# Kernel optimization log

Hardware: AMD Instinct MI355X
Metric: run time of the kernel (lower is better)

## Reference

```python
import jax, jax.numpy as jnp
import numpy as np

MIN_VAL = -1200.0
MAX_VAL = 1000.0


def setup_inputs() -> dict:
    key = jax.random.key(0)
    k1, _ = jax.random.split(key)
    # Scale so values spread across the [-1200, 1000] range; a small tail
    # falls outside the range and must be ignored (torch.histc semantics).
    x = jax.random.normal(k1, (32, 12, 256, 256), dtype=jnp.float32) * 400.0
    hist_counts = jnp.zeros((12, 2200), dtype=jnp.float32)
    return {"x": x, "hist_counts": hist_counts}


def reference(x, hist_counts):
    """Fused multi-channel histogram matching torch.histc per channel.

    torch.histc semantics: `bins` uniform bins over [min, max]; values
    outside [min, max] are ignored; values exactly equal to max land in the
    last bin. Returns updated hist_counts (buffer + batch histogram).
    """
    C, bins = hist_counts.shape
    # [B, C, H, W] -> [C, B*H*W]
    xf = jnp.transpose(x, (1, 0, 2, 3)).reshape(C, -1).astype(jnp.float32)
    scale = bins / (MAX_VAL - MIN_VAL)
    idx = jnp.floor((xf - MIN_VAL) * scale).astype(jnp.int32)
    idx = jnp.clip(idx, 0, bins - 1)  # maps x == MAX_VAL into last bin
    in_range = (xf >= MIN_VAL) & (xf <= MAX_VAL)
    # Flatten channel+bin into one scatter; out-of-range -> dump slot C*bins.
    flat_idx = idx + jnp.arange(C, dtype=jnp.int32)[:, None] * bins
    flat_idx = jnp.where(in_range, flat_idx, C * bins)
    counts = jnp.zeros(C * bins + 1, dtype=jnp.float32).at[flat_idx.ravel()].add(1.0)
    return hist_counts + counts[: C * bins].reshape(C, bins)
```

## Files before the change

### kernel.cpp

```cpp
#include <hip/hip_runtime.h>

#define NCHAN 12
#define NBINS 2200
#define HMIN  (-1200.0f)
#define HMAX  (1000.0f)
#define SLICE_ELEMS 65536
#define SPLIT 4
#define BLOCK 256

__global__ __launch_bounds__(BLOCK)
void init_out(const float* __restrict__ hist, float* __restrict__ out, int n) {
    int i = (blockIdx.x * BLOCK + threadIdx.x) * 4;
    if (i + 3 < n) {
        *(float4*)(out + i) = *(const float4*)(hist + i);
    } else {
        for (; i < n; ++i) out[i] = hist[i];
    }
}

__device__ __forceinline__ void bin4(const float4 v, unsigned int* lh) {
    float vals[4] = {v.x, v.y, v.z, v.w};
#pragma unroll
    for (int j = 0; j < 4; ++j) {
        float t = vals[j] + 1200.0f;
        if (t >= 0.0f && vals[j] <= HMAX) {
            int idx = min((int)t, NBINS - 1);
            atomicAdd(&lh[idx], 1u);
        }
    }
}

__global__ __launch_bounds__(BLOCK)
void hist_kernel(const float* __restrict__ x, float* __restrict__ out) {
    __shared__ unsigned int lh[NBINS];
    for (int i = threadIdx.x; i < NBINS; i += BLOCK) lh[i] = 0u;
    __syncthreads();

    const int slice = blockIdx.x / SPLIT;
    const int sub   = blockIdx.x % SPLIT;
    const int c     = slice % NCHAN;
    const int chunk = SLICE_ELEMS / SPLIT;

    const float4* __restrict__ xp =
        (const float4*)(x + (long long)slice * SLICE_ELEMS + (long long)sub * chunk);

#pragma unroll
    for (int k = 0; k < 2; ++k) {
        const int base = threadIdx.x + k * (BLOCK * 8);
        float4 v[8];
#pragma unroll
        for (int u = 0; u < 8; ++u) v[u] = xp[base + u * BLOCK];
#pragma unroll
        for (int u = 0; u < 8; ++u) bin4(v[u], lh);
    }
    __syncthreads();

    float* __restrict__ outc = out + c * NBINS;
    for (int i = threadIdx.x; i < NBINS; i += BLOCK) {
        unsigned int v = lh[i];
        if (v) atomicAdd(&outc[i], (float)v);
    }
}

extern "C" void kernel_launch(void* const* d_in, const int* in_sizes, int n_in,
                              void* d_out, int out_size, void* d_ws, size_t ws_size,
                              hipStream_t stream) {
    const float* x    = (const float*)d_in[0];
    const float* hist = (const float*)d_in[1];
    float* out        = (float*)d_out;

    int nvec = (out_size + 3) / 4;
    int nblk = (nvec + BLOCK - 1) / BLOCK;
    init_out<<<nblk, BLOCK, 0, stream>>>(hist, out, out_size);

    int nslices = in_sizes[0] / SLICE_ELEMS;
    hist_kernel<<<nslices * SPLIT, BLOCK, 0, stream>>>(x, out);
}
```

Baseline: 148.8 us.

## Replace global float atomics with per-block workspace histograms and a reduction kernel

```diff
diff --git a/kernel.cpp b/kernel.cpp
--- a/kernel.cpp
+++ b/kernel.cpp
@@ -2,21 +2,10 @@
 
 #define NCHAN 12
 #define NBINS 2200
-#define HMIN  (-1200.0f)
 #define HMAX  (1000.0f)
 #define SLICE_ELEMS 65536
 #define SPLIT 4
 #define BLOCK 256
-
-__global__ __launch_bounds__(BLOCK)
-void init_out(const float* __restrict__ hist, float* __restrict__ out, int n) {
-    int i = (blockIdx.x * BLOCK + threadIdx.x) * 4;
-    if (i + 3 < n) {
-        *(float4*)(out + i) = *(const float4*)(hist + i);
-    } else {
-        for (; i < n; ++i) out[i] = hist[i];
-    }
-}
 
 __device__ __forceinline__ void bin4(const float4 v, unsigned int* lh) {
     float vals[4] = {v.x, v.y, v.z, v.w};
@@ -31,14 +20,13 @@
 }
 
 __global__ __launch_bounds__(BLOCK)
-void hist_kernel(const float* __restrict__ x, float* __restrict__ out) {
+void hist_kernel(const float* __restrict__ x, unsigned int* __restrict__ ws) {
     __shared__ unsigned int lh[NBINS];
     for (int i = threadIdx.x; i < NBINS; i += BLOCK) lh[i] = 0u;
     __syncthreads();
 
     const int slice = blockIdx.x / SPLIT;
     const int sub   = blockIdx.x % SPLIT;
-    const int c     = slice % NCHAN;
     const int chunk = SLICE_ELEMS / SPLIT;
 
     const float4* __restrict__ xp =
@@ -55,11 +43,30 @@
     }
     __syncthreads();
 
-    float* __restrict__ outc = out + c * NBINS;
-    for (int i = threadIdx.x; i < NBINS; i += BLOCK) {
-        unsigned int v = lh[i];
-        if (v) atomicAdd(&outc[i], (float)v);
+    unsigned int* __restrict__ wsb = ws + (long long)blockIdx.x * NBINS;
+    for (int i = threadIdx.x; i < NBINS; i += BLOCK) wsb[i] = lh[i];
+}
+
+__global__ __launch_bounds__(BLOCK)
+void reduce_kernel(const unsigned int* __restrict__ ws,
+                   const float* __restrict__ hist,
+                   float* __restrict__ out, int nbatch) {
+    int idx = blockIdx.x * BLOCK + threadIdx.x;
+    if (idx >= NCHAN * NBINS) return;
+    int c   = idx / NBINS;
+    int bin = idx - c * NBINS;
+
+    unsigned int s0 = 0, s1 = 0, s2 = 0, s3 = 0;
+#pragma unroll 4
+    for (int b = 0; b < nbatch; ++b) {
+        const unsigned int* p =
+            ws + (long long)((b * NCHAN + c) * SPLIT) * NBINS + bin;
+        s0 += p[0 * NBINS];
+        s1 += p[1 * NBINS];
+        s2 += p[2 * NBINS];
+        s3 += p[3 * NBINS];
     }
+    out[idx] = hist[idx] + (float)(s0 + s1 + s2 + s3);
 }
 
 extern "C" void kernel_launch(void* const* d_in, const int* in_sizes, int n_in,
@@ -68,11 +75,14 @@
     const float* x    = (const float*)d_in[0];
     const float* hist = (const float*)d_in[1];
     float* out        = (float*)d_out;
-
-    int nvec = (out_size + 3) / 4;
-    int nblk = (nvec + BLOCK - 1) / BLOCK;
-    init_out<<<nblk, BLOCK, 0, stream>>>(hist, out, out_size);
+    unsigned int* ws  = (unsigned int*)d_ws;
 
     int nslices = in_sizes[0] / SLICE_ELEMS;
-    hist_kernel<<<nslices * SPLIT, BLOCK, 0, stream>>>(x, out);
+    int nbatch  = nslices / NCHAN;
+
+    hist_kernel<<<nslices * SPLIT, BLOCK, 0, stream>>>(x, ws);
+
+    int total = NCHAN * NBINS;
+    int nblk  = (total + BLOCK - 1) / BLOCK;
+    reduce_kernel<<<nblk, BLOCK, 0, stream>>>(ws, hist, out, nbatch);
 }
```

Measured after the change: 155.0 us. 1.04x slower.
